# Kernel tuning notes

Measured on AMD Instinct MI355X. Metric: run time of the kernel, lower is better.

## Reference

```python
import jax, jax.numpy as jnp
import numpy as np

B, N, D0 = 128, 128, 512   # batch, n_objects, obj_dim
H, KD, R = 32, 64, 16      # n_heads, key_dim, n_relations
D = D0 + 1                 # with temporal tag

def setup_inputs() -> dict:
    key = jax.random.key(0)
    k1, k2, k3, k4, k5 = jax.random.split(key, 5)
    s = 0.02
    return {
        'obj_seq': jax.random.normal(k1, (B, N, D0), jnp.float32),
        'W_k':  jax.random.normal(k2, (KD, D), jnp.float32) * s,
        'W_q1': jax.random.normal(k3, (H * KD, D * N), jnp.float32) * s,
        'W_q2': jax.random.normal(k4, (H * KD, D * N), jnp.float32) * s,
        'W_s':  jax.random.normal(k5, (R, D), jnp.float32) * s,
    }

def reference(obj_seq, W_k, W_q1, W_q2, W_s):
    b, n, _ = obj_seq.shape
    # append temporal tag channel: obj -> [B, N, D]
    tag = jnp.broadcast_to(jnp.arange(n, dtype=obj_seq.dtype)[None, :, None], (b, n, 1))
    obj = jnp.concatenate([obj_seq, tag], axis=2)
    flat = obj.reshape(b, -1)                      # [B, N*D]
    Q1 = (flat @ W_q1.T).reshape(b, H, KD)         # [B, H, KD]
    Q2 = (flat @ W_q2.T).reshape(b, H, KD)
    K = obj @ W_k.T                                # [B, N, KD]
    # scores [B, N, H], softmax over objects (dim=1 in torch)
    A1 = jax.nn.softmax(jnp.einsum('bhk,bnk->bnh', Q1, K), axis=1)
    A2 = jax.nn.softmax(jnp.einsum('bhk,bnk->bnh', Q2, K), axis=1)
    # attention-weighted object sums: [B, H, D]
    E1 = jnp.einsum('bnh,bnd->bhd', A1, obj)
    E2 = jnp.einsum('bnh,bnd->bhd', A2, obj)
    Dr = E1 @ W_s.T - E2 @ W_s.T                   # [B, H, R]
    Dr = jnp.concatenate([Dr, E1[:, :, -1:], E2[:, :, -1:]], axis=2)  # [B, H, R+2]
    return Dr.reshape(b, -1)                       # [B, H*(R+2)]
```

## Files before the change

kernel.cpp:

```cpp
#include <hip/hip_runtime.h>
#include <cstdint>

typedef _Float16 f16;
typedef _Float16 f16x8 __attribute__((ext_vector_type(8)));
typedef short s16x8 __attribute__((ext_vector_type(8)));
typedef unsigned u32x4 __attribute__((ext_vector_type(4)));
typedef float f32x4 __attribute__((ext_vector_type(4)));
typedef float floatx4 __attribute__((ext_vector_type(4)));

#define KTOT 65664
#define KSTEPS 2052
#define DP 544

__device__ __forceinline__ void gload_lds16(const void* g, void* l) {
  __builtin_amdgcn_global_load_lds(
      (const __attribute__((address_space(1))) void*)g,
      (__attribute__((address_space(3))) void*)l, 16, 0, 0);
}

__device__ __forceinline__ unsigned bfpack(float e0, float e1) {
  return (__float_as_uint(e0) >> 16) | (__float_as_uint(e1) & 0xffff0000u);
}
__device__ __forceinline__ float bfhi(float x) {
  return __uint_as_float(__float_as_uint(x) & 0xffff0000u);
}

__global__ void prep_flat(const float* __restrict__ obj_seq, char* __restrict__ flatA) {
  int o = blockIdx.x * 256 + threadIdx.x;
  int row = o & 127;
  int k8 = (o >> 7) & 3;
  int pl = (o >> 9) & 1;
  int kb = o >> 10;
  int k0 = kb * 32 + k8 * 8;
  unsigned w[4];
#pragma unroll
  for (int j = 0; j < 8; j += 2) {
    float v[2];
#pragma unroll
    for (int jj = 0; jj < 2; ++jj) {
      int k = k0 + j + jj;
      int n = k / 513;
      int d = k - n * 513;
      float x = (d < 512) ? obj_seq[(((size_t)(row << 7) + n) << 9) + d] : (float)n;
      if (pl) x = x - bfhi(x);
      v[jj] = x;
    }
    w[j >> 1] = bfpack(v[0], v[1]);
  }
  *(u32x4*)(flatA + (size_t)o * 16) = (u32x4){w[0], w[1], w[2], w[3]};
}

__global__ void prep_obj(const float* __restrict__ obj_seq, f16* __restrict__ objHi,
                         f16* __restrict__ objLo, f16* __restrict__ objT16) {
  __shared__ f16 tile[32][132];
  int b = blockIdx.x / 17, c = blockIdx.x - 17 * (blockIdx.x / 17);
  int t = threadIdx.x;
  if (c < 16) {
#pragma unroll
    for (int i = 0; i < 16; ++i) {
      int e = t + i * 256;
      int n = e >> 5, dd = e & 31;
      float v = obj_seq[(((size_t)(b << 7) + n) << 9) + (c << 5) + dd];
      f16 h = (f16)v;
      objHi[((size_t)((b << 7) + n)) * DP + (c << 5) + dd] = h;
      objLo[((size_t)((b << 7) + n)) * DP + (c << 5) + dd] = (f16)(v - (float)h);
      tile[dd][n] = h;
    }
    __syncthreads();
#pragma unroll
    for (int i = 0; i < 16; ++i) {
      int e = t + i * 256;
      int dd = e >> 7, n = e & 127;
      objT16[(((size_t)b * DP + (c << 5) + dd) << 7) + n] = tile[dd][n];
    }
  } else {
#pragma unroll
    for (int i = 0; i < 16; ++i) {
      int e = t + i * 256;
      int n = e >> 5, dd = e & 31;
      f16 h = (dd == 0) ? (f16)(float)n : (f16)0.f;
      objHi[((size_t)((b << 7) + n)) * DP + 512 + dd] = h;
      objLo[((size_t)((b << 7) + n)) * DP + 512 + dd] = (f16)0.f;
    }
#pragma unroll
    for (int i = 0; i < 16; ++i) {
      int e = t + i * 256;
      int dd = e >> 7, n = e & 127;
      objT16[(((size_t)b * DP + 512 + dd) << 7) + n] = (dd == 0) ? (f16)(float)n : (f16)0.f;
    }
  }
}

__global__ void prep_wk(const float* __restrict__ W_k, f16* __restrict__ WkHi,
                        f16* __restrict__ WkLo) {
  int o = blockIdx.x * 256 + threadIdx.x;
  int kd = o / DP, d = o - kd * DP;
  float v = (d < 513) ? W_k[kd * 513 + d] * 1024.f : 0.f;
  f16 h = (f16)v;
  WkHi[o] = h;
  WkLo[o] = (f16)(v - (float)h);
}

__global__ __launch_bounds__(512, 2) void qgemm(const char* __restrict__ flatA,
                                                const float* __restrict__ Wq1,
                                                const float* __restrict__ Wq2,
                                                float* __restrict__ Qpart) {
  __shared__ __align__(16) char smem[147456];
  const int tid = threadIdx.x;
  const int lane = tid & 63;
  const int wave = tid >> 6;
  const int wm = wave >> 2, wn = wave & 3;
  const int l15 = lane & 15, lk = lane >> 4;
  const int ntile = blockIdx.x & 15;
  const int ksp = blockIdx.x >> 4;
  const int t0 = ksp * 129;
  const int nt = min(129, KSTEPS - t0);
  const float* Wsrc = (ntile < 8) ? (Wq1 + (size_t)ntile * 256 * KTOT)
                                  : (Wq2 + (size_t)(ntile - 8) * 256 * KTOT);

  const char* asrc = flatA + (size_t)t0 * 16384 + tid * 16;
  const float* wsrcs[4];
#pragma unroll
  for (int c = 0; c < 4; ++c) {
    int col = c * 64 + (tid >> 3);
    int gs = (tid & 7) ^ (col & 7);
    wsrcs[c] = Wsrc + (size_t)col * KTOT + (size_t)t0 * 32 + gs * 4;
  }

  int aoff[2][4];
#pragma unroll
  for (int pl = 0; pl < 2; ++pl)
#pragma unroll
    for (int mi = 0; mi < 4; ++mi)
      aoff[pl][mi] = pl * 8192 + lk * 2048 + (wm * 64 + mi * 16 + l15) * 16;
  int woff[4][2];
#pragma unroll
  for (int nf = 0; nf < 4; ++nf) {
    int col = wn * 64 + nf * 16 + l15;
#pragma unroll
    for (int j = 0; j < 2; ++j)
      woff[nf][j] = col * 128 + (((2 * lk + j) ^ (col & 7)) << 4);
  }

  f32x4 acc[4][4];
#pragma unroll
  for (int mi = 0; mi < 4; ++mi)
#pragma unroll
    for (int nf = 0; nf < 4; ++nf) acc[mi][nf] = (f32x4){0.f, 0.f, 0.f, 0.f};

  auto stageW = [&](int tt, int slot) {
    char* S = smem + 49152 + slot * 32768;
#pragma unroll
    for (int c = 0; c < 4; ++c)
      gload_lds16(wsrcs[c] + (size_t)tt * 32, S + c * 8192 + tid * 16);
  };
  auto stageA = [&](int tt, int slot) {
    char* S = smem + slot * 16384;
    gload_lds16(asrc + (size_t)tt * 16384, S + tid * 16);
    gload_lds16(asrc + (size_t)tt * 16384 + 8192, S + 8192 + tid * 16);
  };

  auto compute = [&](const char* SA, const char* SW) {
    s16x8 wH[4], wL[4];
#pragma unroll
    for (int nf = 0; nf < 4; ++nf) {
      floatx4 a = *(const floatx4*)(SW + woff[nf][0]);
      floatx4 b = *(const floatx4*)(SW + woff[nf][1]);
      u32x4 H = (u32x4){bfpack(a[0], a[1]), bfpack(a[2], a[3]),
                        bfpack(b[0], b[1]), bfpack(b[2], b[3])};
      float l0 = a[0] - bfhi(a[0]), l1 = a[1] - bfhi(a[1]);
      float l2 = a[2] - bfhi(a[2]), l3 = a[3] - bfhi(a[3]);
      float l4 = b[0] - bfhi(b[0]), l5 = b[1] - bfhi(b[1]);
      float l6 = b[2] - bfhi(b[2]), l7 = b[3] - bfhi(b[3]);
      u32x4 L = (u32x4){bfpack(l0, l1), bfpack(l2, l3), bfpack(l4, l5), bfpack(l6, l7)};
      wH[nf] = *(s16x8*)&H;
      wL[nf] = *(s16x8*)&L;
    }
    __builtin_amdgcn_s_setprio(1);
#pragma unroll
    for (int mi = 0; mi < 4; ++mi) {
      s16x8 aH = *(const s16x8*)(SA + aoff[0][mi]);
      s16x8 aL = *(const s16x8*)(SA + aoff[1][mi]);
#pragma unroll
      for (int nf = 0; nf < 4; ++nf) {
        acc[mi][nf] = __builtin_amdgcn_mfma_f32_16x16x32_bf16(aH, wH[nf], acc[mi][nf], 0, 0, 0);
        acc[mi][nf] = __builtin_amdgcn_mfma_f32_16x16x32_bf16(aH, wL[nf], acc[mi][nf], 0, 0, 0);
        acc[mi][nf] = __builtin_amdgcn_mfma_f32_16x16x32_bf16(aL, wH[nf], acc[mi][nf], 0, 0, 0);
      }
    }
    __builtin_amdgcn_s_setprio(0);
  };

  stageW(0, 0); stageA(0, 0);
  stageW(1, 1); stageA(1, 1);

  int sl = 0;
  for (int t = 0; t < nt; ++t) {
    if (t < nt - 2) asm volatile("s_waitcnt vmcnt(6)" ::: "memory");
    else            asm volatile("s_waitcnt vmcnt(0)" ::: "memory");
    __builtin_amdgcn_s_barrier();
    __builtin_amdgcn_sched_barrier(0);
    int s2 = sl + 2; if (s2 >= 3) s2 -= 3;
    if (t + 2 < nt) stageW(t + 2, s2);
    __builtin_amdgcn_sched_barrier(0);
    compute(smem + sl * 16384, smem + 49152 + sl * 32768);
    if (t + 2 < nt) stageA(t + 2, s2);
    sl = (sl == 2) ? 0 : sl + 1;
  }

  float* qout = Qpart + (size_t)ksp * 524288;
#pragma unroll
  for (int mi = 0; mi < 4; ++mi) {
    int row = wm * 64 + mi * 16 + lk * 4;
#pragma unroll
    for (int nf = 0; nf < 4; ++nf) {
      int col = ntile * 256 + wn * 64 + nf * 16 + l15;
#pragma unroll
      for (int j = 0; j < 4; ++j)
        qout[(size_t)(row + j) * 4096 + col] = acc[mi][nf][j];
    }
  }
}

__global__ __launch_bounds__(512, 1) void predinet_tail(
    const f16* __restrict__ objHi, const f16* __restrict__ objLo, const f16* __restrict__ objT16,
    const f16* __restrict__ WkHi, const f16* __restrict__ WkLo,
    const float* __restrict__ Qpart, const float* __restrict__ W_s, float* __restrict__ out) {
  __shared__ __align__(16) char smem[105984];
  const int b = blockIdx.x;
  const int tid = threadIdx.x, lane = tid & 63, wave = tid >> 6;
  const int l15 = lane & 15, lk = lane >> 4;

  f16* WT = (f16*)(smem);
  f16* Qh = (f16*)(smem + 17408);
  f16* Ql = (f16*)(smem + 26624);
  f16* Kh = (f16*)(smem + 35840);
  f16* Kl = (f16*)(smem + 54272);
  float* S = (float*)(smem + 72704);
  f16* E = (f16*)(smem + 17408);
  float* DL = (float*)(smem + 96832);

  {
    const float* qp = Qpart + (size_t)b * 4096 + tid * 8;
    floatx4 q0 = (floatx4){0.f, 0.f, 0.f, 0.f};
    floatx4 q1 = (floatx4){0.f, 0.f, 0.f, 0.f};
#pragma unroll
    for (int p = 0; p < 16; ++p) {
      q0 += *(const floatx4*)(qp + (size_t)p * 524288);
      q1 += *(const floatx4*)(qp + (size_t)p * 524288 + 4);
    }
    int hp = tid >> 3, kd = (tid * 8) & 63;
    f16x8 vh, vl;
#pragma unroll
    for (int j = 0; j < 4; ++j) {
      f16 h0 = (f16)q0[j]; vh[j] = h0; vl[j] = (f16)(q0[j] - (float)h0);
      f16 h1 = (f16)q1[j]; vh[4 + j] = h1; vl[4 + j] = (f16)(q1[j] - (float)h1);
    }
    *(f16x8*)(Qh + hp * 72 + kd) = vh;
    *(f16x8*)(Ql + hp * 72 + kd) = vl;
  }
  {
    f32x4 acc[4];
#pragma unroll
    for (int nf = 0; nf < 4; ++nf) acc[nf] = (f32x4){0.f, 0.f, 0.f, 0.f};
    const f16* arowH = objHi + ((size_t)(b * 128) + wave * 16 + l15) * DP + lk * 8;
    const f16* arowL = objLo + ((size_t)(b * 128) + wave * 16 + l15) * DP + lk * 8;
    const f16* bhi = WkHi + (size_t)l15 * DP + lk * 8;
    const f16* blo = WkLo + (size_t)l15 * DP + lk * 8;
    for (int ks = 0; ks < 17; ++ks) {
      f16x8 ah = *(const f16x8*)(arowH + ks * 32);
      f16x8 al = *(const f16x8*)(arowL + ks * 32);
#pragma unroll
      for (int nf = 0; nf < 4; ++nf) {
        f16x8 h = *(const f16x8*)(bhi + (size_t)nf * 16 * DP + ks * 32);
        f16x8 l = *(const f16x8*)(blo + (size_t)nf * 16 * DP + ks * 32);
        acc[nf] = __builtin_amdgcn_mfma_f32_16x16x32_f16(ah, h, acc[nf], 0, 0, 0);
        acc[nf] = __builtin_amdgcn_mfma_f32_16x16x32_f16(ah, l, acc[nf], 0, 0, 0);
        acc[nf] = __builtin_amdgcn_mfma_f32_16x16x32_f16(al, h, acc[nf], 0, 0, 0);
      }
    }
#pragma unroll
    for (int nf = 0; nf < 4; ++nf)
#pragma unroll
      for (int j = 0; j < 4; ++j) {
        float kv = acc[nf][j] * (1.f / 1024.f);
        f16 h = (f16)kv;
        Kh[(wave * 16 + lk * 4 + j) * 72 + nf * 16 + l15] = h;
        Kl[(wave * 16 + lk * 4 + j) * 72 + nf * 16 + l15] = (f16)(kv - (float)h);
      }
  }
  __syncthreads();
  {
    f32x4 acc[4];
#pragma unroll
    for (int nf = 0; nf < 4; ++nf) acc[nf] = (f32x4){0.f, 0.f, 0.f, 0.f};
#pragma unroll
    for (int ks = 0; ks < 2; ++ks) {
      f16x8 ah = *(const f16x8*)(Kh + (wave * 16 + l15) * 72 + ks * 32 + lk * 8);
      f16x8 al = *(const f16x8*)(Kl + (wave * 16 + l15) * 72 + ks * 32 + lk * 8);
#pragma unroll
      for (int nf = 0; nf < 4; ++nf) {
        f16x8 bh = *(const f16x8*)(Qh + (nf * 16 + l15) * 72 + ks * 32 + lk * 8);
        f16x8 bl = *(const f16x8*)(Ql + (nf * 16 + l15) * 72 + ks * 32 + lk * 8);
        acc[nf] = __builtin_amdgcn_mfma_f32_16x16x32_f16(ah, bh, acc[nf], 0, 0, 0);
        acc[nf] = __builtin_amdgcn_mfma_f32_16x16x32_f16(ah, bl, acc[nf], 0, 0, 0);
        acc[nf] = __builtin_amdgcn_mfma_f32_16x16x32_f16(al, bh, acc[nf], 0, 0, 0);
      }
    }
#pragma unroll
    for (int nf = 0; nf < 4; ++nf)
#pragma unroll
      for (int j = 0; j < 4; ++j)
        S[(wave * 16 + lk * 4 + j) * 65 + nf * 16 + l15] = acc[nf][j];
  }
  __syncthreads();
  {
#pragma unroll
    for (int ci = 0; ci < 8; ++ci) {
      int c = wave * 8 + ci;
      float s0 = S[lane * 65 + c], s1 = S[(lane + 64) * 65 + c];
      float m = fmaxf(s0, s1);
      for (int off = 32; off; off >>= 1) m = fmaxf(m, __shfl_xor(m, off));
      float e0 = __expf(s0 - m), e1 = __expf(s1 - m);
      float sum = e0 + e1;
      for (int off = 32; off; off >>= 1) sum += __shfl_xor(sum, off);
      float inv = 1.f / sum;
      WT[c * 136 + lane] = (f16)(e0 * inv);
      WT[c * 136 + 64 + lane] = (f16)(e1 * inv);
    }
  }
  __syncthreads();
  {
    f16x8 bw[4][4];
#pragma unroll
    for (int nf = 0; nf < 4; ++nf)
#pragma unroll
      for (int ks = 0; ks < 4; ++ks)
        bw[nf][ks] = *(const f16x8*)(WT + (nf * 16 + l15) * 136 + ks * 32 + lk * 8);
    for (int r = 0; r < 5; ++r) {
      int mi = r * 8 + wave;
      if (mi >= 34) break;
      const f16* arow = objT16 + (((size_t)b * DP + mi * 16 + l15) << 7) + lk * 8;
      f16x8 a[4];
#pragma unroll
      for (int ks = 0; ks < 4; ++ks) a[ks] = *(const f16x8*)(arow + ks * 32);
#pragma unroll
      for (int nf = 0; nf < 4; ++nf) {
        f32x4 acc = (f32x4){0.f, 0.f, 0.f, 0.f};
#pragma unroll
        for (int ks = 0; ks < 4; ++ks)
          acc = __builtin_amdgcn_mfma_f32_16x16x32_f16(a[ks], bw[nf][ks], acc, 0, 0, 0);
#pragma unroll
        for (int j = 0; j < 4; ++j)
          E[(mi * 16 + lk * 4 + j) * 73 + nf * 16 + l15] = (f16)acc[j];
      }
    }
  }
  __syncthreads();
  {
    f16* Ws16 = WT;
    for (int i = tid; i < 16 * DP; i += 512) {
      int r = i / DP, d = i - r * DP;
      Ws16[i] = (f16)((d < 513) ? W_s[r * 513 + d] : 0.f);
    }
  }
  __syncthreads();
  if (wave < 4) {
    const f16* Ws16 = WT;
    f32x4 acc = (f32x4){0.f, 0.f, 0.f, 0.f};
    for (int ks = 0; ks < 17; ++ks) {
      f16x8 a = *(const f16x8*)(Ws16 + l15 * DP + ks * 32 + lk * 8);
      f16x8 bv;
#pragma unroll
      for (int jj = 0; jj < 8; ++jj)
        bv[jj] = E[(ks * 32 + lk * 8 + jj) * 73 + wave * 16 + l15];
      acc = __builtin_amdgcn_mfma_f32_16x16x32_f16(a, bv, acc, 0, 0, 0);
    }
#pragma unroll
    for (int j = 0; j < 4; ++j) DL[(lk * 4 + j) * 64 + wave * 16 + l15] = acc[j];
  }
  __syncthreads();
  {
    int h = tid >> 4, r = tid & 15;
    float v = DL[r * 64 + h] - DL[r * 64 + 32 + h];
    out[(size_t)b * 576 + h * 18 + r] = v;
    if (tid < 64) {
      int set = tid >> 5, hh = tid & 31;
      out[(size_t)b * 576 + hh * 18 + 16 + set] = (float)E[512 * 73 + set * 32 + hh];
    }
  }
}

extern "C" void kernel_launch(void* const* d_in, const int* in_sizes, int n_in,
                              void* d_out, int out_size, void* d_ws, size_t ws_size,
                              hipStream_t stream) {
  const float* obj_seq = (const float*)d_in[0];
  const float* W_k = (const float*)d_in[1];
  const float* W_q1 = (const float*)d_in[2];
  const float* W_q2 = (const float*)d_in[3];
  const float* W_s = (const float*)d_in[4];
  float* out = (float*)d_out;

  char* ws = (char*)d_ws;
  size_t off = 0;
  auto carve = [&](size_t bytes) -> char* {
    char* p = ws + off;
    off += (bytes + 255) & ~(size_t)255;
    return p;
  };
  char* flatA = carve((size_t)KSTEPS * 16384);
  f16* objHi = (f16*)carve((size_t)16384 * DP * 2);
  f16* objLo = (f16*)carve((size_t)16384 * DP * 2);
  f16* objT16 = (f16*)carve((size_t)128 * DP * 128 * 2);
  f16* WkHi = (f16*)carve((size_t)64 * DP * 2);
  f16* WkLo = (f16*)carve((size_t)64 * DP * 2);
  float* Qpart = (float*)carve((size_t)16 * 524288 * 4);
  (void)ws_size; (void)in_sizes; (void)n_in; (void)out_size;

  prep_flat<<<8208, 256, 0, stream>>>(obj_seq, flatA);
  prep_obj<<<2176, 256, 0, stream>>>(obj_seq, objHi, objLo, objT16);
  prep_wk<<<136, 256, 0, stream>>>(W_k, WkHi, WkLo);
  qgemm<<<256, 512, 0, stream>>>(flatA, W_q1, W_q2, Qpart);
  predinet_tail<<<128, 512, 0, stream>>>(objHi, objLo, objT16, WkHi, WkLo, Qpart, W_s, out);
}
```

Measured before the change: 350.9 us.

## Replace LDS-staged Q GEMM with direct register-prefetched global loads

The Q projection GEMM no longer stages A and W tiles through shared memory with global_load_lds and barriers. Each wave now loads its own A fragments and fp32 W fragments straight into registers, double-buffered two steps ahead, and splits the bf16 hi/lo inside the MFMA loop. The K-split is also rebalanced evenly across 16 splits instead of fixed 129-step chunks. This removes LDS traffic and block barriers, but raises register pressure and causes redundant global reads of W across waves that share columns, and of A across waves with the same wm.

New measurement: 523.3 us. +49.1%, slower.

```diff
diff --git a/kernel.cpp b/kernel.cpp
--- a/kernel.cpp
+++ b/kernel.cpp
@@ -11,12 +11,6 @@
 #define KTOT 65664
 #define KSTEPS 2052
 #define DP 544
-
-__device__ __forceinline__ void gload_lds16(const void* g, void* l) {
-  __builtin_amdgcn_global_load_lds(
-      (const __attribute__((address_space(1))) void*)g,
-      (__attribute__((address_space(3))) void*)l, 16, 0, 0);
-}
 
 __device__ __forceinline__ unsigned bfpack(float e0, float e1) {
   return (__float_as_uint(e0) >> 16) | (__float_as_uint(e1) & 0xffff0000u);
@@ -105,7 +99,6 @@
                                                 const float* __restrict__ Wq1,
                                                 const float* __restrict__ Wq2,
                                                 float* __restrict__ Qpart) {
-  __shared__ __align__(16) char smem[147456];
   const int tid = threadIdx.x;
   const int lane = tid & 63;
   const int wave = tid >> 6;
@@ -113,34 +106,13 @@
   const int l15 = lane & 15, lk = lane >> 4;
   const int ntile = blockIdx.x & 15;
   const int ksp = blockIdx.x >> 4;
-  const int t0 = ksp * 129;
-  const int nt = min(129, KSTEPS - t0);
+  const int t0 = (KSTEPS * ksp) >> 4;
+  const int nt = ((KSTEPS * (ksp + 1)) >> 4) - t0;
   const float* Wsrc = (ntile < 8) ? (Wq1 + (size_t)ntile * 256 * KTOT)
                                   : (Wq2 + (size_t)(ntile - 8) * 256 * KTOT);
 
-  const char* asrc = flatA + (size_t)t0 * 16384 + tid * 16;
-  const float* wsrcs[4];
-#pragma unroll
-  for (int c = 0; c < 4; ++c) {
-    int col = c * 64 + (tid >> 3);
-    int gs = (tid & 7) ^ (col & 7);
-    wsrcs[c] = Wsrc + (size_t)col * KTOT + (size_t)t0 * 32 + gs * 4;
-  }
-
-  int aoff[2][4];
-#pragma unroll
-  for (int pl = 0; pl < 2; ++pl)
-#pragma unroll
-    for (int mi = 0; mi < 4; ++mi)
-      aoff[pl][mi] = pl * 8192 + lk * 2048 + (wm * 64 + mi * 16 + l15) * 16;
-  int woff[4][2];
-#pragma unroll
-  for (int nf = 0; nf < 4; ++nf) {
-    int col = wn * 64 + nf * 16 + l15;
-#pragma unroll
-    for (int j = 0; j < 2; ++j)
-      woff[nf][j] = col * 128 + (((2 * lk + j) ^ (col & 7)) << 4);
-  }
+  const char* abase = flatA + (size_t)t0 * 16384 + lk * 2048 + (wm * 64 + l15) * 16;
+  const float* wbase = Wsrc + (size_t)(wn * 64 + l15) * KTOT + (size_t)t0 * 32 + lk * 8;
 
   f32x4 acc[4][4];
 #pragma unroll
@@ -148,24 +120,30 @@
 #pragma unroll
     for (int nf = 0; nf < 4; ++nf) acc[mi][nf] = (f32x4){0.f, 0.f, 0.f, 0.f};
 
-  auto stageW = [&](int tt, int slot) {
-    char* S = smem + 49152 + slot * 32768;
-#pragma unroll
-    for (int c = 0; c < 4; ++c)
-      gload_lds16(wsrcs[c] + (size_t)tt * 32, S + c * 8192 + tid * 16);
+  s16x8 Ah0[4], Al0[4], Ah1[4], Al1[4];
+  floatx4 Wa0[4], Wb0[4], Wa1[4], Wb1[4];
+
+  auto loadA = [&](int t, s16x8 (&h)[4], s16x8 (&l)[4]) {
+    const char* p = abase + (size_t)t * 16384;
+#pragma unroll
+    for (int mi = 0; mi < 4; ++mi) {
+      h[mi] = *(const s16x8*)(p + mi * 256);
+      l[mi] = *(const s16x8*)(p + 8192 + mi * 256);
+    }
   };
-  auto stageA = [&](int tt, int slot) {
-    char* S = smem + slot * 16384;
-    gload_lds16(asrc + (size_t)tt * 16384, S + tid * 16);
-    gload_lds16(asrc + (size_t)tt * 16384 + 8192, S + 8192 + tid * 16);
+  auto loadW = [&](int t, floatx4 (&wa)[4], floatx4 (&wb)[4]) {
+    const float* p = wbase + (size_t)t * 32;
+#pragma unroll
+    for (int nf = 0; nf < 4; ++nf) {
+      wa[nf] = *(const floatx4*)(p + (size_t)nf * 16 * KTOT);
+      wb[nf] = *(const floatx4*)(p + (size_t)nf * 16 * KTOT + 4);
+    }
   };
-
-  auto compute = [&](const char* SA, const char* SW) {
-    s16x8 wH[4], wL[4];
+  auto comp = [&](s16x8 (&ah)[4], s16x8 (&al)[4], floatx4 (&wa)[4], floatx4 (&wb)[4], int tw) {
+    const float* p = wbase + (size_t)tw * 32;
 #pragma unroll
     for (int nf = 0; nf < 4; ++nf) {
-      floatx4 a = *(const floatx4*)(SW + woff[nf][0]);
-      floatx4 b = *(const floatx4*)(SW + woff[nf][1]);
+      floatx4 a = wa[nf], b = wb[nf];
       u32x4 H = (u32x4){bfpack(a[0], a[1]), bfpack(a[2], a[3]),
                         bfpack(b[0], b[1]), bfpack(b[2], b[3])};
       float l0 = a[0] - bfhi(a[0]), l1 = a[1] - bfhi(a[1]);
@@ -173,39 +151,31 @@
       float l4 = b[0] - bfhi(b[0]), l5 = b[1] - bfhi(b[1]);
       float l6 = b[2] - bfhi(b[2]), l7 = b[3] - bfhi(b[3]);
       u32x4 L = (u32x4){bfpack(l0, l1), bfpack(l2, l3), bfpack(l4, l5), bfpack(l6, l7)};
-      wH[nf] = *(s16x8*)&H;
-      wL[nf] = *(s16x8*)&L;
-    }
-    __builtin_amdgcn_s_setprio(1);
-#pragma unroll
-    for (int mi = 0; mi < 4; ++mi) {
-      s16x8 aH = *(const s16x8*)(SA + aoff[0][mi]);
-      s16x8 aL = *(const s16x8*)(SA + aoff[1][mi]);
-#pragma unroll
-      for (int nf = 0; nf < 4; ++nf) {
-        acc[mi][nf] = __builtin_amdgcn_mfma_f32_16x16x32_bf16(aH, wH[nf], acc[mi][nf], 0, 0, 0);
-        acc[mi][nf] = __builtin_amdgcn_mfma_f32_16x16x32_bf16(aH, wL[nf], acc[mi][nf], 0, 0, 0);
-        acc[mi][nf] = __builtin_amdgcn_mfma_f32_16x16x32_bf16(aL, wH[nf], acc[mi][nf], 0, 0, 0);
-      }
-    }
-    __builtin_amdgcn_s_setprio(0);
+      wa[nf] = *(const floatx4*)(p + (size_t)nf * 16 * KTOT);
+      wb[nf] = *(const floatx4*)(p + (size_t)nf * 16 * KTOT + 4);
+      s16x8 wH = *(s16x8*)&H;
+      s16x8 wL = *(s16x8*)&L;
+#pragma unroll
+      for (int mi = 0; mi < 4; ++mi) {
+        acc[mi][nf] = __builtin_amdgcn_mfma_f32_16x16x32_bf16(ah[mi], wH, acc[mi][nf], 0, 0, 0);
+        acc[mi][nf] = __builtin_amdgcn_mfma_f32_16x16x32_bf16(ah[mi], wL, acc[mi][nf], 0, 0, 0);
+        acc[mi][nf] = __builtin_amdgcn_mfma_f32_16x16x32_bf16(al[mi], wH, acc[mi][nf], 0, 0, 0);
+      }
+    }
   };
 
-  stageW(0, 0); stageA(0, 0);
-  stageW(1, 1); stageA(1, 1);
-
-  int sl = 0;
-  for (int t = 0; t < nt; ++t) {
-    if (t < nt - 2) asm volatile("s_waitcnt vmcnt(6)" ::: "memory");
-    else            asm volatile("s_waitcnt vmcnt(0)" ::: "memory");
-    __builtin_amdgcn_s_barrier();
-    __builtin_amdgcn_sched_barrier(0);
-    int s2 = sl + 2; if (s2 >= 3) s2 -= 3;
-    if (t + 2 < nt) stageW(t + 2, s2);
-    __builtin_amdgcn_sched_barrier(0);
-    compute(smem + sl * 16384, smem + 49152 + sl * 32768);
-    if (t + 2 < nt) stageA(t + 2, s2);
-    sl = (sl == 2) ? 0 : sl + 1;
+  loadW(0, Wa0, Wb0);
+  loadW((1 < nt) ? 1 : 0, Wa1, Wb1);
+  loadA(0, Ah0, Al0);
+
+  int t = 0;
+  while (true) {
+    { int ta = (t + 1 < nt) ? t + 1 : nt - 1; loadA(ta, Ah1, Al1); }
+    { int tw = (t + 2 < nt) ? t + 2 : nt - 1; comp(Ah0, Al0, Wa0, Wb0, tw); }
+    if (++t >= nt) break;
+    { int ta = (t + 1 < nt) ? t + 1 : nt - 1; loadA(ta, Ah0, Al0); }
+    { int tw = (t + 2 < nt) ? t + 2 : nt - 1; comp(Ah1, Al1, Wa1, Wb1, tw); }
+    if (++t >= nt) break;
   }
 
   float* qout = Qpart + (size_t)ksp * 524288;
```
